# Performance work log

Measured on AMD Instinct MI355X. Metric: run time of the kernel, lower is better.

## Reference

```python
import jax, jax.numpy as jnp
import numpy as np

B, L, H, OUT = 128, 256, 512, 256


def setup_inputs() -> dict:
    key = jax.random.key(0)
    ks = jax.random.split(key, 13)
    s = 1.0 / np.sqrt(H)
    u = lambda k, shape: jax.random.uniform(k, shape, jnp.float32, -s, s)
    C = jax.random.normal(ks[0], (L, H), jnp.float32)
    # strictly increasing observation times per sample
    dt0 = jax.random.uniform(ks[1], (B, L, 1), jnp.float32)
    t = jnp.cumsum(dt0, axis=1)
    mask = jax.random.randint(ks[2], (B, L, H), 0, 2).astype(jnp.int32)
    # GRU-D parameters: fused gate weights [z | r | candidate]
    Wx = u(ks[3], (H, 3 * H))   # input -> gates
    Wh = u(ks[4], (H, 3 * H))   # hidden -> gates
    Wm = u(ks[5], (H, 3 * H))   # mask  -> gates
    b = u(ks[6], (3 * H,))
    w_gx = u(ks[7], (H,))       # diagonal input-decay weight
    b_gx = u(ks[8], (H,))
    W_gh = u(ks[9], (H, H))     # hidden-decay weight
    b_gh = u(ks[10], (H,))
    W_out = u(ks[11], (H, OUT))
    b_out = u(ks[12], (OUT,))
    return dict(C=C, t=t, mask=mask, Wx=Wx, Wh=Wh, Wm=Wm, b=b, w_gx=w_gx,
                b_gx=b_gx, W_gh=W_gh, b_gh=b_gh, W_out=W_out, b_out=b_out)


def _grud_decode(C, t, mask_f, Wx, Wh, Wm, b, w_gx, b_gx, W_gh, b_gh, W_out, b_out):
    Bn, Ln = t.shape[0], t.shape[1]
    Hn = C.shape[1]
    m = mask_f                                                     # (B,L,H) float 0/1
    tt = jnp.broadcast_to(t[:, :, 0:1], (Bn, Ln, Hn))              # (B,L,H)
    dt = tt - jnp.concatenate([tt[:, :1], tt[:, :-1]], axis=1)     # dt[:,0]=0
    x = jnp.broadcast_to(C[None], (Bn, Ln, Hn))
    # empirical mean of observed values per sample/feature
    x_mean = jnp.sum(m * x, axis=1) / jnp.maximum(jnp.sum(m, axis=1), 1.0)  # (B,H)

    def step(carry, inp):
        h, x_last, d_prev, m_prev = carry
        xi, mi, dti = inp                                          # xi:(H,), mi/dti:(B,H)
        # time since last observation (GRU-D delta recurrence)
        delta = dti + (1.0 - m_prev) * d_prev
        gamma_x = jnp.exp(-jnp.maximum(0.0, w_gx * delta + b_gx))  # input decay
        gamma_h = jnp.exp(-jnp.maximum(0.0, delta @ W_gh + b_gh))  # hidden decay
        x_hat = mi * xi + (1.0 - mi) * (gamma_x * x_last + (1.0 - gamma_x) * x_mean)
        h = gamma_h * h
        pre = x_hat @ Wx + mi @ Wm + b                             # (B,3H)
        zr = jax.nn.sigmoid(pre[:, :2 * Hn] + h @ Wh[:, :2 * Hn])
        z, r = zr[:, :Hn], zr[:, Hn:]
        h_tilde = jnp.tanh(pre[:, 2 * Hn:] + (r * h) @ Wh[:, 2 * Hn:])
        h_new = (1.0 - z) * h + z * h_tilde
        x_last = mi * xi + (1.0 - mi) * x_last
        return (h_new, x_last, delta, mi), h_new

    init = (jnp.zeros((Bn, Hn), C.dtype), x_mean,
            jnp.zeros((Bn, Hn), C.dtype), jnp.ones((Bn, Hn), C.dtype))
    xs = (C, jnp.transpose(m, (1, 0, 2)), jnp.transpose(dt, (1, 0, 2)))
    _, h_seq = jax.lax.scan(step, init, xs)                        # (L,B,H)
    h_seq = jnp.transpose(h_seq, (1, 0, 2))                        # (B,L,H) == permute(1,0,2)
    return h_seq @ W_out + b_out                                   # (B,L,OUT)


def reference(C, t, mask, Wx, Wh, Wm, b, w_gx, b_gx, W_gh, b_gh, W_out, b_out):
    return _grud_decode(C, t, mask.astype(C.dtype), Wx, Wh, Wm, b,
                        w_gx, b_gx, W_gh, b_gh, W_out, b_out)
```

## Files before the change

kernel.cpp:

```cpp
#include <hip/hip_runtime.h>
#include <hip/hip_bf16.h>
#include <hip/hip_fp16.h>
#include <stdint.h>

typedef short bf16x8 __attribute__((ext_vector_type(8)));
typedef unsigned short u16x8 __attribute__((ext_vector_type(8)));
typedef float f32x4  __attribute__((ext_vector_type(4)));
typedef __hip_bfloat16 bf16;
typedef unsigned long long u64;

#define MFMA16(a,b,c) __builtin_amdgcn_mfma_f32_16x16x32_bf16((a),(b),(c),0,0,0)

__device__ __forceinline__ float bf2f(bf16 x){ return __bfloat162float(x); }
__device__ __forceinline__ bf16  f2bf(float x){ return __float2bfloat16(x); }
__device__ __forceinline__ short f2bs(float x){ bf16 t = __float2bfloat16(x); return *(short*)&t; }
__device__ __forceinline__ float bs2f(short s){ bf16 t; *(short*)&t = s; return __bfloat162float(t); }
__device__ __forceinline__ float h2f(unsigned short u){ __half t; *(unsigned short*)&t = u; return __half2float(t); }
__device__ __forceinline__ float sf(float x){ return (fabsf(x) < 1e30f) ? x : 0.f; }

#define NB   128
#define NL   256
#define CH   32
#define MCH  4096
#define NQ   8


__global__ void build_wcatT(const float* __restrict__ Wx, const float* __restrict__ Wm,
                            bf16* __restrict__ dst) {
    int i = blockIdx.x * 256 + threadIdx.x;
    if (i >= 1536 * 1024) return;
    int n = i >> 10, k = i & 1023;
    float v = (k < 512) ? Wx[k * 1536 + n] : Wm[(k - 512) * 1536 + n];
    dst[i] = f2bf(sf(v));
}

__global__ void transpose_f2b(const float* __restrict__ src, bf16* __restrict__ dst,
                              int R, int C) {
    int i = blockIdx.x * 256 + threadIdx.x;
    if (i >= R * C) return;
    int r = i % R, c = i / R;
    dst[i] = f2bf(sf(src[r * C + c]));
}


__global__ void xmean_kernel(const int* __restrict__ mask, const float* __restrict__ Cmat,
                             float* __restrict__ xmean) {
    int g = blockIdx.x * 256 + threadIdx.x;
    int b = g >> 9, h = g & 511;
    float s = 0.f, cnt = 0.f;
    for (int l = 0; l < NL; ++l) {
        int m = mask[(size_t)((b << 8) + l) * 512 + h];
        if (m) { s += sf(Cmat[(l << 9) + h]); cnt += 1.f; }
    }
    xmean[g] = s / fmaxf(cnt, 1.f);
}

__global__ void prep_kernel(const int* __restrict__ mask, const float* __restrict__ Cmat,
                            const float* __restrict__ t_in,
                            const float* __restrict__ w_gx, const float* __restrict__ b_gx,
                            const float* __restrict__ xmean,
                            float* __restrict__ xlastC, float* __restrict__ dprevC,
                            float* __restrict__ mprevC, float* __restrict__ tprevC,
                            bf16* __restrict__ Xcat,
                            bf16* __restrict__ Dbuf,
                            int q) {
    int g = blockIdx.x * 256 + threadIdx.x;
    int b = g >> 9, h = g & 511;
    float wg = sf(w_gx[h]), bg = sf(b_gx[h]);
    float xm = xmean[g];
    float xlast, dprev, mprev, tprev;
    if (q == 0) { xlast = xm; dprev = 0.f; mprev = 1.f; tprev = 0.f; }
    else { xlast = xlastC[g]; dprev = dprevC[g]; mprev = mprevC[g]; tprev = tprevC[g]; }
    for (int ll = 0; ll < CH; ++ll) {
        int l = q * CH + ll;
        float tc = sf(t_in[(b << 8) + l]);
        float dtv = (l == 0) ? 0.f : (tc - tprev);
        tprev = tc;
        float mi = (float)mask[(size_t)((b << 8) + l) * 512 + h];
        float delta = dtv + (1.f - mprev) * dprev;
        float gx = __expf(-fmaxf(wg * delta + bg, 0.f));
        float xi = sf(Cmat[(l << 9) + h]);
        float xh = mi * xi + (1.f - mi) * (gx * xlast + (1.f - gx) * xm);
        size_t row = (size_t)ll * 128 + b;
        Xcat[row * 1024 + h]       = f2bf(xh);
        Xcat[row * 1024 + 512 + h] = f2bf(mi);
        Dbuf[row * 512 + h]        = f2bf(delta);
        xlast = mi * xi + (1.f - mi) * xlast;
        dprev = delta; mprev = mi;
    }
    xlastC[g] = xlast; dprevC[g] = dprev; mprevC[g] = mprev; tprevC[g] = tprev;
}

template <int MODE>
__global__ __launch_bounds__(256) void gemm_bt(const bf16* __restrict__ A,
                                               const bf16* __restrict__ BT,
                                               const float* __restrict__ bias,
                                               void* __restrict__ Cout,
                                               int N, int K, int q) {
    const int nb = N >> 7;
    int bn = blockIdx.x % nb, bm = blockIdx.x / nb;
    __shared__ bf16 As[4096];
    __shared__ bf16 Bs[4096];
    int tid = threadIdx.x, lane = tid & 63, w = tid >> 6;
    int wm = w >> 1, wn = w & 1;
    int quad = lane >> 4, l15 = lane & 15;
    f32x4 acc[4][4];
// ... 36 lines not shown
    int row0 = bm * 128 + wm * 64, col0 = bn * 128 + wn * 64;
    #pragma unroll
    for (int mt = 0; mt < 4; ++mt) {
        #pragma unroll
        for (int nt = 0; nt < 4; ++nt) {
            int col = col0 + nt * 16 + l15;
            float bvf = sf(bias[col]);
            #pragma unroll
            for (int r = 0; r < 4; ++r) {
                int row = row0 + mt * 16 + quad * 4 + r;
                float v = acc[mt][nt][r] + bvf;
                if (MODE == 1)
                    ((__half*)Cout)[(size_t)row * N + col] = __float2half(__expf(-fmaxf(v, 0.f)));
                else if (MODE == 2) {
                    int bb = row & 127, lloc = row >> 7;
                    ((float*)Cout)[(size_t)((bb << 8) + q * CH + lloc) * N + col] = v;
                } else
                    ((bf16*)Cout)[(size_t)row * N + col] = f2bf(v);
            }
        }
    }
}

__global__ __launch_bounds__(512, 1) void scan_kernel(
        const bf16* __restrict__ pre,
        const __half* __restrict__ gammaf,
        const bf16* __restrict__ WhT,
        bf16* __restrict__ hseq,
        float* __restrict__ hcarry,
        u64* __restrict__ rbuf,
        u64* __restrict__ hnbuf,
        unsigned* __restrict__ ctr) {
    int bx = blockIdx.x;
    int c = bx & 7, w = bx >> 3;
    int tid = threadIdx.x, lane = tid & 63, v = tid >> 6;
    int wi = (w << 3) | v;
    int quad = lane >> 4, l15 = lane & 15;
    __shared__ bf16 hb[16 * 520];
    __shared__ bf16 rh[16 * 520];

    bf16x8 whz[16], whr[16], whh[16];
    int col0 = wi * 16;
    #pragma unroll
    for (int kf = 0; kf < 16; ++kf) {
        int n = col0 + l15;
        whz[kf] = *(const bf16x8*)(WhT + (size_t)n * 512 + kf * 32 + quad * 8);
        whr[kf] = *(const bf16x8*)(WhT + (size_t)(512 + n) * 512 + kf * 32 + quad * 8);
        whh[kf] = *(const bf16x8*)(WhT + (size_t)(1024 + n) * 512 + kf * 32 + quad * 8);
    }

    u64* rclu = rbuf  + (size_t)c * 2048;
    u64* hclu = hnbuf + (size_t)c * 2048;
    const unsigned short* gus = (const unsigned short*)gammaf;
    unsigned* fA = ctr + c * 64;
    unsigned* fB = ctr + c * 64 + 32;

    for (int i = tid; i < 16 * 512; i += 512) {
        int row = i >> 9, col = i & 511;
        int brow = c * 16 + row;
        float g0 = __half2float(gammaf[(size_t)brow * 512 + col]);
        hb[row * 520 + col] = f2bf(hcarry[(size_t)brow * 512 + col] * g0);
    }
    float hfo[4];
    #pragma unroll
    for (int r = 0; r < 4; ++r) {
        int brow = c * 16 + quad * 4 + r;
        int cc = col0 + l15;
        float g0 = __half2float(gammaf[(size_t)brow * 512 + cc]);
        hfo[r] = hcarry[(size_t)brow * 512 + cc] * g0;
    }
    __syncthreads();

    int rrow = tid >> 5, rword = tid & 31;
    int prow = tid >> 5, pc16 = tid & 31, pcol = pc16 << 4, pregion = pc16 >> 3;

    for (int t = 0; t < CH; ++t) {
        unsigned ep = (unsigned)(t + 1);
        bool lastt = (t == CH - 1);
        float pz[4], prr[4], ph[4], gow[4];
        #pragma unroll
        for (int r = 0; r < 4; ++r) {
            int brow = c * 16 + quad * 4 + r;
            size_t pb = ((size_t)t * 128 + brow) * 1536;
            int cc = col0 + l15;
            pz[r]  = bf2f(pre[pb + cc]);
            prr[r] = bf2f(pre[pb + 512 + cc]);
            ph[r]  = bf2f(pre[pb + 1024 + cc]);
            gow[r] = lastt ? 1.f
                   : __half2float(gammaf[((size_t)(t + 1) * 128 + brow) * 512 + cc]);
        }
        u16x8 gt[2];
        {
            size_t gb = ((size_t)(lastt ? t : t + 1) * 128 + c * 16 + prow) * 512 + pcol;
            #pragma unroll
            for (int j = 0; j < 2; ++j) gt[j] = *(const u16x8*)(gus + gb + j * 8);
        }
        f32x4 az = (f32x4){0.f,0.f,0.f,0.f}, ar = az;
        #pragma unroll
        for (int kf = 0; kf < 16; ++kf) {
            bf16x8 a = *(const bf16x8*)&hb[l15 * 520 + kf * 32 + quad * 8];
            az = MFMA16(a, whz[kf], az);
            ar = MFMA16(a, whr[kf], ar);
        }
        float zv[4];
        #pragma unroll
        for (int r = 0; r < 4; ++r) {
            zv[r] = 1.f / (1.f + __expf(-(az[r] + pz[r])));
            float rv = 1.f / (1.f + __expf(-(ar[r] + prr[r])));
            rh[(quad * 4 + r) * 520 + col0 + l15] = f2bf(rv * hfo[r]);
        }
        __syncthreads();
        {
            u64 wv = *(const u64*)&rh[rrow * 520 + w * 128 + rword * 4];
            __hip_atomic_store(&rclu[rrow * 128 + w * 32 + rword], wv,
                               __ATOMIC_RELAXED, __HIP_MEMORY_SCOPE_AGENT);
        }
        __syncthreads();
        if (tid == 0) {
            __hip_atomic_store(&fA[w], ep, __ATOMIC_RELAXED, __HIP_MEMORY_SCOPE_AGENT);
            int guard = 0;
            for (;;) {
                bool ok = true;
                #pragma unroll
                for (int j = 0; j < 4; ++j)
                    ok &= (__hip_atomic_load(&fA[j], __ATOMIC_RELAXED,
                                             __HIP_MEMORY_SCOPE_AGENT) >= ep);
                if (ok || ++guard >= (1 << 16)) break;
                __builtin_amdgcn_s_sleep(1);
            }
        }
        __syncthreads();
        if (pregion != w) {
            #pragma unroll
            for (int j = 0; j < 4; ++j) {
                u64 wv = __hip_atomic_load(&rclu[prow * 128 + pc16 * 4 + j],
                                           __ATOMIC_RELAXED, __HIP_MEMORY_SCOPE_AGENT);
                *(u64*)&rh[prow * 520 + pcol + j * 4] = wv;
            }
        }
        __syncthreads();
        f32x4 ah = (f32x4){0.f,0.f,0.f,0.f};
        #pragma unroll
        for (int kf = 0; kf < 16; ++kf) {
            bf16x8 a = *(const bf16x8*)&rh[l15 * 520 + kf * 32 + quad * 8];
            ah = MFMA16(a, whh[kf], ah);
        }
        #pragma unroll
        for (int r = 0; r < 4; ++r) {
            int row = quad * 4 + r;
            int cc = col0 + l15;
            float x = ah[r] + ph[r];
            float e = __expf(-2.f * fabsf(x));
            float th = copysignf((1.f - e) / (1.f + e), x);
            float hn = (1.f - zv[r]) * hfo[r] + zv[r] * th;
            hb[row * 520 + cc] = f2bf(hn);
            if (lastt) {
                int brow = c * 16 + row;
                __builtin_nontemporal_store(hn, &hcarry[(size_t)brow * 512 + cc]);
            }
            hfo[r] = hn * gow[r];
        }
        __syncthreads();
        {
            u64 wv = *(const u64*)&hb[rrow * 520 + w * 128 + rword * 4];
            __hip_atomic_store(&hclu[rrow * 128 + w * 32 + rword], wv,
                               __ATOMIC_RELAXED, __HIP_MEMORY_SCOPE_AGENT);
        }
        __syncthreads();
        if (tid == 0) {
            __hip_atomic_store(&fB[w], ep, __ATOMIC_RELAXED, __HIP_MEMORY_SCOPE_AGENT);
            int guard = 0;
            for (;;) {
                bool ok = true;
                #pragma unroll
                for (int j = 0; j < 4; ++j)
                    ok &= (__hip_atomic_load(&fB[j], __ATOMIC_RELAXED,
                                             __HIP_MEMORY_SCOPE_AGENT) >= ep);
                if (ok || ++guard >= (1 << 16)) break;
                __builtin_amdgcn_s_sleep(1);
            }
        }
        __syncthreads();
        u64 hw[4];
        if (pregion != w) {
            #pragma unroll
            for (int j = 0; j < 4; ++j)
                hw[j] = __hip_atomic_load(&hclu[prow * 128 + pc16 * 4 + j],
                                          __ATOMIC_RELAXED, __HIP_MEMORY_SCOPE_AGENT);
        } else {
            #pragma unroll
            for (int j = 0; j < 4; ++j)
                hw[j] = *(const u64*)&hb[prow * 520 + pcol + j * 4];
        }
        if (w == 0) {
            int brow = c * 16 + prow;
            u64* hs = (u64*)&hseq[((size_t)t * 128 + brow) * 512 + pcol];
            #pragma unroll
            for (int j = 0; j < 4; ++j) __builtin_nontemporal_store(hw[j], &hs[j]);
        }
        #pragma unroll
        for (int j = 0; j < 4; ++j) {
            u16x8* gp = (u16x8*)&gt[0];
            short o4[4];
            #pragma unroll
            for (int e = 0; e < 4; ++e) {
                short hv = (short)((hw[j] >> (16 * e)) & 0xFFFF);
                float g = lastt ? 1.f : h2f(((unsigned short*)gp)[j * 4 + e]);
                o4[e] = f2bs(bs2f(hv) * g);
            }
            u64 ov = ((u64)(unsigned short)o4[0]) | ((u64)(unsigned short)o4[1] << 16)
                   | ((u64)(unsigned short)o4[2] << 32) | ((u64)(unsigned short)o4[3] << 48);
            *(u64*)&hb[prow * 520 + pcol + j * 4] = ov;
        }
        __syncthreads();
    }
}


extern "C" void kernel_launch(void* const* d_in, const int* in_sizes, int n_in,
                              void* d_out, int out_size, void* d_ws, size_t ws_size,
                              hipStream_t stream) {
    const float* C     = (const float*)d_in[0];
    const float* t_in  = (const float*)d_in[1];
    const int*   mask  = (const int*)d_in[2];
    const float* Wx    = (const float*)d_in[3];
    const float* Wh    = (const float*)d_in[4];
    const float* Wm    = (const float*)d_in[5];
    const float* bvec  = (const float*)d_in[6];
    const float* w_gx  = (const float*)d_in[7];
    const float* b_gx  = (const float*)d_in[8];
    const float* W_gh  = (const float*)d_in[9];
    const float* b_gh  = (const float*)d_in[10];
    const float* W_out = (const float*)d_in[11];
    const float* b_out = (const float*)d_in[12];

    char* w = (char*)d_ws;
    unsigned* ctr   = (unsigned*)(w + 0);
    float* hcarry   = (float*)(w + 16384);
    float* xmean    = (float*)(w + 278528);
    float* xlastC   = (float*)(w + 540672);
    float* dprevC   = (float*)(w + 802816);
    float* mprevC   = (float*)(w + 1064960);
    float* tprevC   = (float*)(w + 1327104);
    bf16*  wcatT    = (bf16*)(w + 1589248);
    bf16*  wghT     = (bf16*)(w + 4734976);
    bf16*  whT      = (bf16*)(w + 5259264);
    bf16*  woutT    = (bf16*)(w + 6832128);
    bf16*  Xcat     = (bf16*)(w + 7094272);
    bf16*  Dbuf     = (bf16*)(w + 15482880);
    bf16*  pre      = (bf16*)(w + 19677184);
    __half* gamma   = (__half*)(w + 32260096);
    bf16*  hseq     = (bf16*)(w + 36454400);
    u64*   rbuf     = (u64*)(w + 40648704);
    u64*   hnbuf    = (u64*)(w + 40779776);

    hipMemsetAsync(w, 0, 278528, stream);

    build_wcatT<<<6144, 256, 0, stream>>>(Wx, Wm, wcatT);
    transpose_f2b<<<1024, 256, 0, stream>>>(W_gh, wghT, 512, 512);
    transpose_f2b<<<3072, 256, 0, stream>>>(Wh, whT, 512, 1536);
    transpose_f2b<<<512, 256, 0, stream>>>(W_out, woutT, 512, 256);
    xmean_kernel<<<256, 256, 0, stream>>>(mask, C, xmean);

    for (int q = 0; q < NQ; ++q) {
        prep_kernel<<<256, 256, 0, stream>>>(mask, C, t_in, w_gx, b_gx, xmean,
                                             xlastC, dprevC, mprevC, tprevC,
                                             Xcat, Dbuf, q);
        gemm_bt<0><<<32 * 12, 256, 0, stream>>>(Xcat, wcatT, bvec, (void*)pre, 1536, 1024, q);
        gemm_bt<1><<<32 * 4, 256, 0, stream>>>(Dbuf, wghT, b_gh, (void*)gamma, 512, 512, q);
        scan_kernel<<<32, 512, 0, stream>>>(pre, gamma, whT, hseq, hcarry,
                                            rbuf, hnbuf, ctr + q * 512);
        gemm_bt<2><<<32 * 2, 256, 0, stream>>>(hseq, woutT, b_out, d_out, 256, 512, q);
    }
}
```

Baseline: 2.884 ms.

## Overlap cluster barrier waits with local z-gate and partial candidate MFMAs

The r-gate is now computed first so its exchange can be published early. While waiting on the cross-block flag, each block computes the z-gate MFMAs and the locally owned slice of the candidate matmul, so only the remote K-chunks remain after the barrier. The per-step loads of pre-activations and gamma for the next step are issued before the second barrier wait, and the local h-region rescale is done before the wait too. The intent is to hide inter-workgroup synchronisation latency behind useful compute, at the cost of more live registers and more complex control flow.

```diff
diff --git a/kernel.cpp b/kernel.cpp
--- a/kernel.cpp
+++ b/kernel.cpp
@@ -23,6 +23,8 @@
 #define CH   32
 #define MCH  4096
 #define NQ   8
+
+#define RLXA __ATOMIC_RELAXED, __HIP_MEMORY_SCOPE_AGENT
 
 
 __global__ void build_wcatT(const float* __restrict__ Wx, const float* __restrict__ Wm,
@@ -216,57 +218,70 @@
     int rrow = tid >> 5, rword = tid & 31;
     int prow = tid >> 5, pc16 = tid & 31, pcol = pc16 << 4, pregion = pc16 >> 3;
 
-    for (int t = 0; t < CH; ++t) {
-        unsigned ep = (unsigned)(t + 1);
-        bool lastt = (t == CH - 1);
-        float pz[4], prr[4], ph[4], gow[4];
+    float pz[4], prr[4], ph[4], gow[4];
+    u16x8 gt[2], gtn[2];
+    {
         #pragma unroll
         for (int r = 0; r < 4; ++r) {
             int brow = c * 16 + quad * 4 + r;
-            size_t pb = ((size_t)t * 128 + brow) * 1536;
+            size_t pb = (size_t)brow * 1536;
             int cc = col0 + l15;
             pz[r]  = bf2f(pre[pb + cc]);
             prr[r] = bf2f(pre[pb + 512 + cc]);
             ph[r]  = bf2f(pre[pb + 1024 + cc]);
-            gow[r] = lastt ? 1.f
-                   : __half2float(gammaf[((size_t)(t + 1) * 128 + brow) * 512 + cc]);
-        }
-        u16x8 gt[2];
+            gow[r] = __half2float(gammaf[((size_t)128 + brow) * 512 + cc]);
+        }
+        size_t gb = ((size_t)128 + c * 16 + prow) * 512 + pcol;
+        gt[0] = *(const u16x8*)(gus + gb);
+        gt[1] = *(const u16x8*)(gus + gb + 8);
+    }
+
+    for (int t = 0; t < CH; ++t) {
+        unsigned ep = (unsigned)(t + 1);
+        bool lastt = (t == CH - 1);
+
+        f32x4 ar = (f32x4){0.f,0.f,0.f,0.f};
+        #pragma unroll
+        for (int kf = 0; kf < 16; ++kf) {
+            bf16x8 a = *(const bf16x8*)&hb[l15 * 520 + kf * 32 + quad * 8];
+            ar = MFMA16(a, whr[kf], ar);
+        }
+        #pragma unroll
+        for (int r = 0; r < 4; ++r) {
+            float rv = 1.f / (1.f + __expf(-(ar[r] + prr[r])));
+            rh[(quad * 4 + r) * 520 + col0 + l15] = f2bf(rv * hfo[r]);
+        }
+        __syncthreads();
         {
-            size_t gb = ((size_t)(lastt ? t : t + 1) * 128 + c * 16 + prow) * 512 + pcol;
-            #pragma unroll
-            for (int j = 0; j < 2; ++j) gt[j] = *(const u16x8*)(gus + gb + j * 8);
-        }
-        f32x4 az = (f32x4){0.f,0.f,0.f,0.f}, ar = az;
+            u64 wv = *(const u64*)&rh[rrow * 520 + w * 128 + rword * 4];
+            __hip_atomic_store(&rclu[rrow * 128 + w * 32 + rword], wv, RLXA);
+        }
+        __syncthreads();
+        if (tid == 0) __hip_atomic_store(&fA[w], ep, RLXA);
+        f32x4 az = (f32x4){0.f,0.f,0.f,0.f};
         #pragma unroll
         for (int kf = 0; kf < 16; ++kf) {
             bf16x8 a = *(const bf16x8*)&hb[l15 * 520 + kf * 32 + quad * 8];
             az = MFMA16(a, whz[kf], az);
-            ar = MFMA16(a, whr[kf], ar);
+        }
+        f32x4 ah = (f32x4){0.f,0.f,0.f,0.f};
+        #pragma unroll
+        for (int kq = 0; kq < 4; ++kq) {
+            int kf = w * 4 + kq;
+            bf16x8 a = *(const bf16x8*)&rh[l15 * 520 + kf * 32 + quad * 8];
+            ah = MFMA16(a, whh[kf], ah);
         }
         float zv[4];
         #pragma unroll
-        for (int r = 0; r < 4; ++r) {
+        for (int r = 0; r < 4; ++r)
             zv[r] = 1.f / (1.f + __expf(-(az[r] + pz[r])));
-            float rv = 1.f / (1.f + __expf(-(ar[r] + prr[r])));
-            rh[(quad * 4 + r) * 520 + col0 + l15] = f2bf(rv * hfo[r]);
-        }
-        __syncthreads();
-        {
-            u64 wv = *(const u64*)&rh[rrow * 520 + w * 128 + rword * 4];
-            __hip_atomic_store(&rclu[rrow * 128 + w * 32 + rword], wv,
-                               __ATOMIC_RELAXED, __HIP_MEMORY_SCOPE_AGENT);
-        }
-        __syncthreads();
         if (tid == 0) {
-            __hip_atomic_store(&fA[w], ep, __ATOMIC_RELAXED, __HIP_MEMORY_SCOPE_AGENT);
             int guard = 0;
             for (;;) {
                 bool ok = true;
                 #pragma unroll
                 for (int j = 0; j < 4; ++j)
-                    ok &= (__hip_atomic_load(&fA[j], __ATOMIC_RELAXED,
-                                             __HIP_MEMORY_SCOPE_AGENT) >= ep);
+                    ok &= (__hip_atomic_load(&fA[j], RLXA) >= ep);
                 if (ok || ++guard >= (1 << 16)) break;
                 __builtin_amdgcn_s_sleep(1);
             }
@@ -275,15 +290,14 @@
         if (pregion != w) {
             #pragma unroll
             for (int j = 0; j < 4; ++j) {
-                u64 wv = __hip_atomic_load(&rclu[prow * 128 + pc16 * 4 + j],
-                                           __ATOMIC_RELAXED, __HIP_MEMORY_SCOPE_AGENT);
+                u64 wv = __hip_atomic_load(&rclu[prow * 128 + pc16 * 4 + j], RLXA);
                 *(u64*)&rh[prow * 520 + pcol + j * 4] = wv;
             }
         }
         __syncthreads();
-        f32x4 ah = (f32x4){0.f,0.f,0.f,0.f};
         #pragma unroll
         for (int kf = 0; kf < 16; ++kf) {
+            if ((kf >> 2) == w) continue;
             bf16x8 a = *(const bf16x8*)&rh[l15 * 520 + kf * 32 + quad * 8];
             ah = MFMA16(a, whh[kf], ah);
         }
@@ -305,56 +319,99 @@
         __syncthreads();
         {
             u64 wv = *(const u64*)&hb[rrow * 520 + w * 128 + rword * 4];
-            __hip_atomic_store(&hclu[rrow * 128 + w * 32 + rword], wv,
-                               __ATOMIC_RELAXED, __HIP_MEMORY_SCOPE_AGENT);
-        }
-        __syncthreads();
+            __hip_atomic_store(&hclu[rrow * 128 + w * 32 + rword], wv, RLXA);
+        }
+        __syncthreads();
+        if (tid == 0) __hip_atomic_store(&fB[w], ep, RLXA);
+        if (pregion == w) {
+            u64 h0 = *(const u64*)&hb[prow * 520 + pcol + 0];
+            u64 h1 = *(const u64*)&hb[prow * 520 + pcol + 4];
+            u64 h2 = *(const u64*)&hb[prow * 520 + pcol + 8];
+            u64 h3 = *(const u64*)&hb[prow * 520 + pcol + 12];
+            if (w == 0) {
+                int brow = c * 16 + prow;
+                u64* hs = (u64*)&hseq[((size_t)t * 128 + brow) * 512 + pcol];
+                __builtin_nontemporal_store(h0, &hs[0]);
+                __builtin_nontemporal_store(h1, &hs[1]);
+                __builtin_nontemporal_store(h2, &hs[2]);
+                __builtin_nontemporal_store(h3, &hs[3]);
+            }
+            const unsigned short* gtu = (const unsigned short*)&gt[0];
+            u64 hwv[4] = {h0, h1, h2, h3};
+            #pragma unroll
+            for (int j = 0; j < 4; ++j) {
+                short o4[4];
+                #pragma unroll
+                for (int e = 0; e < 4; ++e) {
+                    short hv = (short)((hwv[j] >> (16 * e)) & 0xFFFF);
+                    float g = lastt ? 1.f : h2f(gtu[j * 4 + e]);
+                    o4[e] = f2bs(bs2f(hv) * g);
+                }
+                u64 ov = ((u64)(unsigned short)o4[0]) | ((u64)(unsigned short)o4[1] << 16)
+                       | ((u64)(unsigned short)o4[2] << 32) | ((u64)(unsigned short)o4[3] << 48);
+                *(u64*)&hb[prow * 520 + pcol + j * 4] = ov;
+            }
+        }
+        if (!lastt) {
+            int tn = t + 1; bool lastn = (tn == CH - 1);
+            #pragma unroll
+            for (int r = 0; r < 4; ++r) {
+                int brow = c * 16 + quad * 4 + r;
+                size_t pb = ((size_t)tn * 128 + brow) * 1536;
+                int cc = col0 + l15;
+                pz[r]  = bf2f(pre[pb + cc]);
+                prr[r] = bf2f(pre[pb + 512 + cc]);
+                ph[r]  = bf2f(pre[pb + 1024 + cc]);
+                gow[r] = lastn ? 1.f
+                       : __half2float(gammaf[((size_t)(tn + 1) * 128 + brow) * 512 + cc]);
+            }
+            size_t gb = ((size_t)(lastn ? tn : tn + 1) * 128 + c * 16 + prow) * 512 + pcol;
+            gtn[0] = *(const u16x8*)(gus + gb);
+            gtn[1] = *(const u16x8*)(gus + gb + 8);
+        }
         if (tid == 0) {
-            __hip_atomic_store(&fB[w], ep, __ATOMIC_RELAXED, __HIP_MEMORY_SCOPE_AGENT);
             int guard = 0;
             for (;;) {
                 bool ok = true;
                 #pragma unroll
                 for (int j = 0; j < 4; ++j)
-                    ok &= (__hip_atomic_load(&fB[j], __ATOMIC_RELAXED,
-                                             __HIP_MEMORY_SCOPE_AGENT) >= ep);
+                    ok &= (__hip_atomic_load(&fB[j], RLXA) >= ep);
                 if (ok || ++guard >= (1 << 16)) break;
                 __builtin_amdgcn_s_sleep(1);
             }
         }
         __syncthreads();
-        u64 hw[4];
         if (pregion != w) {
-            #pragma unroll
-            for (int j = 0; j < 4; ++j)
-                hw[j] = __hip_atomic_load(&hclu[prow * 128 + pc16 * 4 + j],
-                                          __ATOMIC_RELAXED, __HIP_MEMORY_SCOPE_AGENT);
-        } else {
-            #pragma unroll
-            for (int j = 0; j < 4; ++j)
-                hw[j] = *(const u64*)&hb[prow * 520 + pcol + j * 4];
-        }
-        if (w == 0) {
-            int brow = c * 16 + prow;
-            u64* hs = (u64*)&hseq[((size_t)t * 128 + brow) * 512 + pcol];
-            #pragma unroll
-            for (int j = 0; j < 4; ++j) __builtin_nontemporal_store(hw[j], &hs[j]);
-        }
-        #pragma unroll
-        for (int j = 0; j < 4; ++j) {
-            u16x8* gp = (u16x8*)&gt[0];
-            short o4[4];
-            #pragma unroll
-            for (int e = 0; e < 4; ++e) {
-                short hv = (short)((hw[j] >> (16 * e)) & 0xFFFF);
-                float g = lastt ? 1.f : h2f(((unsigned short*)gp)[j * 4 + e]);
-                o4[e] = f2bs(bs2f(hv) * g);
-            }
-            u64 ov = ((u64)(unsigned short)o4[0]) | ((u64)(unsigned short)o4[1] << 16)
-                   | ((u64)(unsigned short)o4[2] << 32) | ((u64)(unsigned short)o4[3] << 48);
-            *(u64*)&hb[prow * 520 + pcol + j * 4] = ov;
-        }
-        __syncthreads();
+            u64 h0 = __hip_atomic_load(&hclu[prow * 128 + pc16 * 4 + 0], RLXA);
+            u64 h1 = __hip_atomic_load(&hclu[prow * 128 + pc16 * 4 + 1], RLXA);
+            u64 h2 = __hip_atomic_load(&hclu[prow * 128 + pc16 * 4 + 2], RLXA);
+            u64 h3 = __hip_atomic_load(&hclu[prow * 128 + pc16 * 4 + 3], RLXA);
+            if (w == 0) {
+                int brow = c * 16 + prow;
+                u64* hs = (u64*)&hseq[((size_t)t * 128 + brow) * 512 + pcol];
+                __builtin_nontemporal_store(h0, &hs[0]);
+                __builtin_nontemporal_store(h1, &hs[1]);
+                __builtin_nontemporal_store(h2, &hs[2]);
+                __builtin_nontemporal_store(h3, &hs[3]);
+            }
+            const unsigned short* gtu = (const unsigned short*)&gt[0];
+            u64 hwv[4] = {h0, h1, h2, h3};
+            #pragma unroll
+            for (int j = 0; j < 4; ++j) {
+                short o4[4];
+                #pragma unroll
+                for (int e = 0; e < 4; ++e) {
+                    short hv = (short)((hwv[j] >> (16 * e)) & 0xFFFF);
+                    float g = lastt ? 1.f : h2f(gtu[j * 4 + e]);
+                    o4[e] = f2bs(bs2f(hv) * g);
+                }
+                u64 ov = ((u64)(unsigned short)o4[0]) | ((u64)(unsigned short)o4[1] << 16)
+                       | ((u64)(unsigned short)o4[2] << 32) | ((u64)(unsigned short)o4[3] << 48);
+                *(u64*)&hb[prow * 520 + pcol + j * 4] = ov;
+            }
+        }
+        __syncthreads();
+        if (!lastt) { gt[0] = gtn[0]; gt[1] = gtn[1]; }
     }
 }
 
```

Result: slower. 3.326 ms (+15.3%).

## Hoist full-sequence prep and GEMMs out of chunk loop; swizzle LDS layout

Applied to the files above, without the earlier changes.

When the workspace is large enough, the input prep, the gate GEMM, the decay GEMM and the output GEMM each run once over all 256 timesteps instead of in 8 chunks. The scan kernel then runs per chunk over the full-size buffers. This cuts launch count and gives the GEMMs far larger grids. The shared-memory h/rh tiles also move from padded row-major to a blocked layout that matches the MFMA operand reads, aiming to cut LDS bank conflicts. The fast path needs about 275 MB of workspace and falls back to the chunked path otherwise.

```diff
diff --git a/kernel.cpp b/kernel.cpp
--- a/kernel.cpp
+++ b/kernel.cpp
@@ -21,8 +21,13 @@
 #define NB   128
 #define NL   256
 #define CH   32
-#define MCH  4096
 #define NQ   8
+
+#define RLXA __ATOMIC_RELAXED, __HIP_MEMORY_SCOPE_AGENT
+
+__device__ __forceinline__ int lx(int row, int col) {
+    return ((col >> 5) << 9) | (((col >> 3) & 3) << 7) | (row << 3) | (col & 7);
+}
 
 
 __global__ void build_wcatT(const float* __restrict__ Wx, const float* __restrict__ Wm,
@@ -63,7 +68,7 @@
                             float* __restrict__ mprevC, float* __restrict__ tprevC,
                             bf16* __restrict__ Xcat,
                             bf16* __restrict__ Dbuf,
-                            int q) {
+                            int q, int nsteps) {
     int g = blockIdx.x * 256 + threadIdx.x;
     int b = g >> 9, h = g & 511;
     float wg = sf(w_gx[h]), bg = sf(b_gx[h]);
@@ -71,7 +76,7 @@
     float xlast, dprev, mprev, tprev;
     if (q == 0) { xlast = xm; dprev = 0.f; mprev = 1.f; tprev = 0.f; }
     else { xlast = xlastC[g]; dprev = dprevC[g]; mprev = mprevC[g]; tprev = tprevC[g]; }
-    for (int ll = 0; ll < CH; ++ll) {
+    for (int ll = 0; ll < nsteps; ++ll) {
         int l = q * CH + ll;
         float tc = sf(t_in[(b << 8) + l]);
         float dtv = (l == 0) ? 0.f : (tc - tprev);
@@ -178,8 +183,8 @@
     int tid = threadIdx.x, lane = tid & 63, v = tid >> 6;
     int wi = (w << 3) | v;
     int quad = lane >> 4, l15 = lane & 15;
-    __shared__ bf16 hb[16 * 520];
-    __shared__ bf16 rh[16 * 520];
+    __shared__ bf16 hb[8192];
+    __shared__ bf16 rh[8192];
 
     bf16x8 whz[16], whr[16], whh[16];
     int col0 = wi * 16;
@@ -201,7 +206,7 @@
         int row = i >> 9, col = i & 511;
         int brow = c * 16 + row;
         float g0 = __half2float(gammaf[(size_t)brow * 512 + col]);
-        hb[row * 520 + col] = f2bf(hcarry[(size_t)brow * 512 + col] * g0);
+        hb[lx(row, col)] = f2bf(hcarry[(size_t)brow * 512 + col] * g0);
     }
     float hfo[4];
     #pragma unroll
@@ -214,6 +219,8 @@
     __syncthreads();
 
     int rrow = tid >> 5, rword = tid & 31;
+    int rcol = w * 128 + rword * 4;
+    int rsrc = lx(rrow, rcol);
     int prow = tid >> 5, pc16 = tid & 31, pcol = pc16 << 4, pregion = pc16 >> 3;
 
     for (int t = 0; t < CH; ++t) {
@@ -240,7 +247,7 @@
         f32x4 az = (f32x4){0.f,0.f,0.f,0.f}, ar = az;
         #pragma unroll
         for (int kf = 0; kf < 16; ++kf) {
-            bf16x8 a = *(const bf16x8*)&hb[l15 * 520 + kf * 32 + quad * 8];
+            bf16x8 a = *(const bf16x8*)&hb[(kf << 9) | (quad << 7) | (l15 << 3)];
             az = MFMA16(a, whz[kf], az);
             ar = MFMA16(a, whr[kf], ar);
         }
@@ -249,24 +256,22 @@
         for (int r = 0; r < 4; ++r) {
             zv[r] = 1.f / (1.f + __expf(-(az[r] + pz[r])));
             float rv = 1.f / (1.f + __expf(-(ar[r] + prr[r])));
-            rh[(quad * 4 + r) * 520 + col0 + l15] = f2bf(rv * hfo[r]);
+            rh[lx(quad * 4 + r, col0 + l15)] = f2bf(rv * hfo[r]);
         }
         __syncthreads();
         {
-            u64 wv = *(const u64*)&rh[rrow * 520 + w * 128 + rword * 4];
-            __hip_atomic_store(&rclu[rrow * 128 + w * 32 + rword], wv,
-                               __ATOMIC_RELAXED, __HIP_MEMORY_SCOPE_AGENT);
+            u64 wv = *(const u64*)&rh[rsrc];
+            __hip_atomic_store(&rclu[rrow * 128 + w * 32 + rword], wv, RLXA);
         }
         __syncthreads();
         if (tid == 0) {
-            __hip_atomic_store(&fA[w], ep, __ATOMIC_RELAXED, __HIP_MEMORY_SCOPE_AGENT);
+            __hip_atomic_store(&fA[w], ep, RLXA);
             int guard = 0;
             for (;;) {
                 bool ok = true;
                 #pragma unroll
                 for (int j = 0; j < 4; ++j)
-                    ok &= (__hip_atomic_load(&fA[j], __ATOMIC_RELAXED,
-                                             __HIP_MEMORY_SCOPE_AGENT) >= ep);
+                    ok &= (__hip_atomic_load(&fA[j], RLXA) >= ep);
                 if (ok || ++guard >= (1 << 16)) break;
                 __builtin_amdgcn_s_sleep(1);
             }
@@ -275,16 +280,15 @@
         if (pregion != w) {
             #pragma unroll
             for (int j = 0; j < 4; ++j) {
-                u64 wv = __hip_atomic_load(&rclu[prow * 128 + pc16 * 4 + j],
-                                           __ATOMIC_RELAXED, __HIP_MEMORY_SCOPE_AGENT);
-                *(u64*)&rh[prow * 520 + pcol + j * 4] = wv;
+                u64 wv = __hip_atomic_load(&rclu[prow * 128 + pc16 * 4 + j], RLXA);
+                *(u64*)&rh[lx(prow, pcol + j * 4)] = wv;
             }
         }
         __syncthreads();
         f32x4 ah = (f32x4){0.f,0.f,0.f,0.f};
         #pragma unroll
         for (int kf = 0; kf < 16; ++kf) {
-            bf16x8 a = *(const bf16x8*)&rh[l15 * 520 + kf * 32 + quad * 8];
+            bf16x8 a = *(const bf16x8*)&rh[(kf << 9) | (quad << 7) | (l15 << 3)];
             ah = MFMA16(a, whh[kf], ah);
         }
         #pragma unroll
@@ -295,7 +299,7 @@
             float e = __expf(-2.f * fabsf(x));
             float th = copysignf((1.f - e) / (1.f + e), x);
             float hn = (1.f - zv[r]) * hfo[r] + zv[r] * th;
-            hb[row * 520 + cc] = f2bf(hn);
+            hb[lx(row, cc)] = f2bf(hn);
             if (lastt) {
                 int brow = c * 16 + row;
                 __builtin_nontemporal_store(hn, &hcarry[(size_t)brow * 512 + cc]);
@@ -304,20 +308,18 @@
         }
         __syncthreads();
         {
-            u64 wv = *(const u64*)&hb[rrow * 520 + w * 128 + rword * 4];
-            __hip_atomic_store(&hclu[rrow * 128 + w * 32 + rword], wv,
-                               __ATOMIC_RELAXED, __HIP_MEMORY_SCOPE_AGENT);
+            u64 wv = *(const u64*)&hb[rsrc];
+            __hip_atomic_store(&hclu[rrow * 128 + w * 32 + rword], wv, RLXA);
         }
         __syncthreads();
         if (tid == 0) {
-            __hip_atomic_store(&fB[w], ep, __ATOMIC_RELAXED, __HIP_MEMORY_SCOPE_AGENT);
+            __hip_atomic_store(&fB[w], ep, RLXA);
             int guard = 0;
             for (;;) {
                 bool ok = true;
                 #pragma unroll
                 for (int j = 0; j < 4; ++j)
-                    ok &= (__hip_atomic_load(&fB[j], __ATOMIC_RELAXED,
-                                             __HIP_MEMORY_SCOPE_AGENT) >= ep);
+                    ok &= (__hip_atomic_load(&fB[j], RLXA) >= ep);
                 if (ok || ++guard >= (1 << 16)) break;
                 __builtin_amdgcn_s_sleep(1);
             }
@@ -327,12 +329,11 @@
         if (pregion != w) {
             #pragma unroll
             for (int j = 0; j < 4; ++j)
-                hw[j] = __hip_atomic_load(&hclu[prow * 128 + pc16 * 4 + j],
-                                          __ATOMIC_RELAXED, __HIP_MEMORY_SCOPE_AGENT);
+                hw[j] = __hip_atomic_load(&hclu[prow * 128 + pc16 * 4 + j], RLXA);
         } else {
             #pragma unroll
             for (int j = 0; j < 4; ++j)
-                hw[j] = *(const u64*)&hb[prow * 520 + pcol + j * 4];
+                hw[j] = *(const u64*)&hb[lx(prow, pcol + j * 4)];
         }
         if (w == 0) {
             int brow = c * 16 + prow;
@@ -352,7 +353,7 @@
             }
             u64 ov = ((u64)(unsigned short)o4[0]) | ((u64)(unsigned short)o4[1] << 16)
                    | ((u64)(unsigned short)o4[2] << 32) | ((u64)(unsigned short)o4[3] << 48);
-            *(u64*)&hb[prow * 520 + pcol + j * 4] = ov;
+            *(u64*)&hb[lx(prow, pcol + j * 4)] = ov;
         }
         __syncthreads();
     }
@@ -388,13 +389,6 @@
     bf16*  wghT     = (bf16*)(w + 4734976);
     bf16*  whT      = (bf16*)(w + 5259264);
     bf16*  woutT    = (bf16*)(w + 6832128);
-    bf16*  Xcat     = (bf16*)(w + 7094272);
-    bf16*  Dbuf     = (bf16*)(w + 15482880);
-    bf16*  pre      = (bf16*)(w + 19677184);
-    __half* gamma   = (__half*)(w + 32260096);
-    bf16*  hseq     = (bf16*)(w + 36454400);
-    u64*   rbuf     = (u64*)(w + 40648704);
-    u64*   hnbuf    = (u64*)(w + 40779776);
 
     hipMemsetAsync(w, 0, 278528, stream);
 
@@ -404,14 +398,47 @@
     transpose_f2b<<<512, 256, 0, stream>>>(W_out, woutT, 512, 256);
     xmean_kernel<<<256, 256, 0, stream>>>(mask, C, xmean);
 
-    for (int q = 0; q < NQ; ++q) {
+    const size_t BIG_NEEDED = 275791872ull;
+    if (ws_size >= BIG_NEEDED) {
+        bf16*  XcatF  = (bf16*)(w + 7094272);
+        bf16*  DbufF  = (bf16*)(w + 74203136);
+        bf16*  preF   = (bf16*)(w + 107757568);
+        __half* gamF  = (__half*)(w + 208420864);
+        bf16*  hseqF  = (bf16*)(w + 241975296);
+        u64*   rbuf   = (u64*)(w + 275529728);
+        u64*   hnbuf  = (u64*)(w + 275660800);
+
         prep_kernel<<<256, 256, 0, stream>>>(mask, C, t_in, w_gx, b_gx, xmean,
                                              xlastC, dprevC, mprevC, tprevC,
-                                             Xcat, Dbuf, q);
-        gemm_bt<0><<<32 * 12, 256, 0, stream>>>(Xcat, wcatT, bvec, (void*)pre, 1536, 1024, q);
-        gemm_bt<1><<<32 * 4, 256, 0, stream>>>(Dbuf, wghT, b_gh, (void*)gamma, 512, 512, q);
-        scan_kernel<<<32, 512, 0, stream>>>(pre, gamma, whT, hseq, hcarry,
-                                            rbuf, hnbuf, ctr + q * 512);
-        gemm_bt<2><<<32 * 2, 256, 0, stream>>>(hseq, woutT, b_out, d_out, 256, 512, q);
-    }
-}
+                                             XcatF, DbufF, 0, NL);
+        gemm_bt<0><<<256 * 12, 256, 0, stream>>>(XcatF, wcatT, bvec, (void*)preF, 1536, 1024, 0);
+        gemm_bt<1><<<256 * 4, 256, 0, stream>>>(DbufF, wghT, b_gh, (void*)gamF, 512, 512, 0);
+        for (int q = 0; q < NQ; ++q) {
+            scan_kernel<<<32, 512, 0, stream>>>(preF + (size_t)q * 4096 * 1536,
+                                                gamF + (size_t)q * 4096 * 512,
+                                                whT,
+                                                hseqF + (size_t)q * 4096 * 512,
+                                                hcarry, rbuf, hnbuf, ctr + q * 512);
+        }
+        gemm_bt<2><<<256 * 2, 256, 0, stream>>>(hseqF, woutT, b_out, d_out, 256, 512, 0);
+    } else {
+        bf16*  Xcat   = (bf16*)(w + 7094272);
+        bf16*  Dbuf   = (bf16*)(w + 15482880);
+        bf16*  pre    = (bf16*)(w + 19677184);
+        __half* gamma = (__half*)(w + 32260096);
+        bf16*  hseq   = (bf16*)(w + 36454400);
+        u64*   rbuf   = (u64*)(w + 40648704);
+        u64*   hnbuf  = (u64*)(w + 40779776);
+
+        for (int q = 0; q < NQ; ++q) {
+            prep_kernel<<<256, 256, 0, stream>>>(mask, C, t_in, w_gx, b_gx, xmean,
+                                                 xlastC, dprevC, mprevC, tprevC,
+                                                 Xcat, Dbuf, q, CH);
+            gemm_bt<0><<<32 * 12, 256, 0, stream>>>(Xcat, wcatT, bvec, (void*)pre, 1536, 1024, q);
+            gemm_bt<1><<<32 * 4, 256, 0, stream>>>(Dbuf, wghT, b_gh, (void*)gamma, 512, 512, q);
+            scan_kernel<<<32, 512, 0, stream>>>(pre, gamma, whT, hseq, hcarry,
+                                                rbuf, hnbuf, ctr + q * 512);
+            gemm_bt<2><<<32 * 2, 256, 0, stream>>>(hseq, woutT, b_out, d_out, 256, 512, q);
+        }
+    }
+}
```

Result: slower. 3.192 ms (+10.7%).

## Interleave two batch groups per scan block to hide cross-block flag waits

Applied to the files above, without the earlier changes.

Each scan workgroup now processes two 16-row batch groups (X and Y) instead of one, with the grid halved from 32 to 16 blocks. Phases of the two groups are interleaved so that while one group waits on the inter-block flag exchange for r*h or h_new, the other group's MFMA work and stores proceed. This is meant to hide the latency of the spin-wait synchronisation across the 4 column-split blocks. In exchange, each block does twice the sequential work, uses twice the LDS and more registers, and the flag layout changes.

```diff
diff --git a/kernel.cpp b/kernel.cpp
--- a/kernel.cpp
+++ b/kernel.cpp
@@ -23,6 +23,8 @@
 #define CH   32
 #define MCH  4096
 #define NQ   8
+
+#define RLXA __ATOMIC_RELAXED, __HIP_MEMORY_SCOPE_AGENT
 
 
 __global__ void build_wcatT(const float* __restrict__ Wx, const float* __restrict__ Wm,
@@ -174,12 +176,14 @@
         u64* __restrict__ hnbuf,
         unsigned* __restrict__ ctr) {
     int bx = blockIdx.x;
-    int c = bx & 7, w = bx >> 3;
+    int c = bx & 3, w = bx >> 2;
     int tid = threadIdx.x, lane = tid & 63, v = tid >> 6;
     int wi = (w << 3) | v;
     int quad = lane >> 4, l15 = lane & 15;
-    __shared__ bf16 hb[16 * 520];
-    __shared__ bf16 rh[16 * 520];
+    __shared__ bf16 hbX[16 * 520];
+    __shared__ bf16 rhX[16 * 520];
+    __shared__ bf16 hbY[16 * 520];
+    __shared__ bf16 rhY[16 * 520];
 
     bf16x8 whz[16], whr[16], whh[16];
     int col0 = wi * 16;
@@ -191,25 +195,34 @@
         whh[kf] = *(const bf16x8*)(WhT + (size_t)(1024 + n) * 512 + kf * 32 + quad * 8);
     }
 
-    u64* rclu = rbuf  + (size_t)c * 2048;
-    u64* hclu = hnbuf + (size_t)c * 2048;
+    u64* rcluX = rbuf  + (size_t)(c * 2 + 0) * 2048;
+    u64* rcluY = rbuf  + (size_t)(c * 2 + 1) * 2048;
+    u64* hcluX = hnbuf + (size_t)(c * 2 + 0) * 2048;
+    u64* hcluY = hnbuf + (size_t)(c * 2 + 1) * 2048;
     const unsigned short* gus = (const unsigned short*)gammaf;
-    unsigned* fA = ctr + c * 64;
-    unsigned* fB = ctr + c * 64 + 32;
+    unsigned* fAX = ctr + c * 128;
+    unsigned* fAY = ctr + c * 128 + 8;
+    unsigned* fBX = ctr + c * 128 + 16;
+    unsigned* fBY = ctr + c * 128 + 24;
+    int rowX0 = c * 32, rowY0 = c * 32 + 16;
 
     for (int i = tid; i < 16 * 512; i += 512) {
         int row = i >> 9, col = i & 511;
-        int brow = c * 16 + row;
-        float g0 = __half2float(gammaf[(size_t)brow * 512 + col]);
-        hb[row * 520 + col] = f2bf(hcarry[(size_t)brow * 512 + col] * g0);
-    }
-    float hfo[4];
+        int bX = rowX0 + row, bY = rowY0 + row;
+        hbX[row * 520 + col] = f2bf(hcarry[(size_t)bX * 512 + col]
+                                    * __half2float(gammaf[(size_t)bX * 512 + col]));
+        hbY[row * 520 + col] = f2bf(hcarry[(size_t)bY * 512 + col]
+                                    * __half2float(gammaf[(size_t)bY * 512 + col]));
+    }
+    float hfoX[4], hfoY[4];
     #pragma unroll
     for (int r = 0; r < 4; ++r) {
-        int brow = c * 16 + quad * 4 + r;
+        int bX = rowX0 + quad * 4 + r, bY = rowY0 + quad * 4 + r;
         int cc = col0 + l15;
-        float g0 = __half2float(gammaf[(size_t)brow * 512 + cc]);
-        hfo[r] = hcarry[(size_t)brow * 512 + cc] * g0;
+        hfoX[r] = hcarry[(size_t)bX * 512 + cc]
+                * __half2float(gammaf[(size_t)bX * 512 + cc]);
+        hfoY[r] = hcarry[(size_t)bY * 512 + cc]
+                * __half2float(gammaf[(size_t)bY * 512 + cc]);
     }
     __syncthreads();
 
@@ -219,54 +232,82 @@
     for (int t = 0; t < CH; ++t) {
         unsigned ep = (unsigned)(t + 1);
         bool lastt = (t == CH - 1);
-        float pz[4], prr[4], ph[4], gow[4];
+        float pzX[4], prrX[4], phX[4], gowX[4];
+        float pzY[4], prrY[4], phY[4], gowY[4];
         #pragma unroll
         for (int r = 0; r < 4; ++r) {
-            int brow = c * 16 + quad * 4 + r;
-            size_t pb = ((size_t)t * 128 + brow) * 1536;
+            int bX = rowX0 + quad * 4 + r, bY = rowY0 + quad * 4 + r;
             int cc = col0 + l15;
-            pz[r]  = bf2f(pre[pb + cc]);
-            prr[r] = bf2f(pre[pb + 512 + cc]);
-            ph[r]  = bf2f(pre[pb + 1024 + cc]);
-            gow[r] = lastt ? 1.f
-                   : __half2float(gammaf[((size_t)(t + 1) * 128 + brow) * 512 + cc]);
-        }
-        u16x8 gt[2];
-        {
-            size_t gb = ((size_t)(lastt ? t : t + 1) * 128 + c * 16 + prow) * 512 + pcol;
-            #pragma unroll
-            for (int j = 0; j < 2; ++j) gt[j] = *(const u16x8*)(gus + gb + j * 8);
-        }
-        f32x4 az = (f32x4){0.f,0.f,0.f,0.f}, ar = az;
+            size_t pbX = ((size_t)t * 128 + bX) * 1536;
+            size_t pbY = ((size_t)t * 128 + bY) * 1536;
+            pzX[r]  = bf2f(pre[pbX + cc]);
+            prrX[r] = bf2f(pre[pbX + 512 + cc]);
+            phX[r]  = bf2f(pre[pbX + 1024 + cc]);
+            pzY[r]  = bf2f(pre[pbY + cc]);
+            prrY[r] = bf2f(pre[pbY + 512 + cc]);
+            phY[r]  = bf2f(pre[pbY + 1024 + cc]);
+            gowX[r] = lastt ? 1.f
+                    : __half2float(gammaf[((size_t)(t + 1) * 128 + bX) * 512 + cc]);
+            gowY[r] = lastt ? 1.f
+                    : __half2float(gammaf[((size_t)(t + 1) * 128 + bY) * 512 + cc]);
+        }
+        u16x8 gtX[2], gtY[2];
+        {
+            size_t gstep = (size_t)(lastt ? t : t + 1) * 128;
+            size_t gbX = (gstep + rowX0 + prow) * 512 + pcol;
+            size_t gbY = (gstep + rowY0 + prow) * 512 + pcol;
+            gtX[0] = *(const u16x8*)(gus + gbX); gtX[1] = *(const u16x8*)(gus + gbX + 8);
+            gtY[0] = *(const u16x8*)(gus + gbY); gtY[1] = *(const u16x8*)(gus + gbY + 8);
+        }
+        f32x4 azX = (f32x4){0.f,0.f,0.f,0.f}, arX = azX;
         #pragma unroll
         for (int kf = 0; kf < 16; ++kf) {
-            bf16x8 a = *(const bf16x8*)&hb[l15 * 520 + kf * 32 + quad * 8];
-            az = MFMA16(a, whz[kf], az);
-            ar = MFMA16(a, whr[kf], ar);
-        }
-        float zv[4];
+            bf16x8 a = *(const bf16x8*)&hbX[l15 * 520 + kf * 32 + quad * 8];
+            azX = MFMA16(a, whz[kf], azX);
+            arX = MFMA16(a, whr[kf], arX);
+        }
+        float zvX[4];
         #pragma unroll
         for (int r = 0; r < 4; ++r) {
-            zv[r] = 1.f / (1.f + __expf(-(az[r] + pz[r])));
-            float rv = 1.f / (1.f + __expf(-(ar[r] + prr[r])));
-            rh[(quad * 4 + r) * 520 + col0 + l15] = f2bf(rv * hfo[r]);
-        }
-        __syncthreads();
-        {
-            u64 wv = *(const u64*)&rh[rrow * 520 + w * 128 + rword * 4];
-            __hip_atomic_store(&rclu[rrow * 128 + w * 32 + rword], wv,
-                               __ATOMIC_RELAXED, __HIP_MEMORY_SCOPE_AGENT);
-        }
-        __syncthreads();
+            zvX[r] = 1.f / (1.f + __expf(-(azX[r] + pzX[r])));
+            float rv = 1.f / (1.f + __expf(-(arX[r] + prrX[r])));
+            rhX[(quad * 4 + r) * 520 + col0 + l15] = f2bf(rv * hfoX[r]);
+        }
+        __syncthreads();
+        {
+            u64 wv = *(const u64*)&rhX[rrow * 520 + w * 128 + rword * 4];
+            __hip_atomic_store(&rcluX[rrow * 128 + w * 32 + rword], wv, RLXA);
+        }
+        __syncthreads();
+        if (tid == 0) __hip_atomic_store(&fAX[w], ep, RLXA);
+        f32x4 azY = (f32x4){0.f,0.f,0.f,0.f}, arY = azY;
+        #pragma unroll
+        for (int kf = 0; kf < 16; ++kf) {
+            bf16x8 a = *(const bf16x8*)&hbY[l15 * 520 + kf * 32 + quad * 8];
+            azY = MFMA16(a, whz[kf], azY);
+            arY = MFMA16(a, whr[kf], arY);
+        }
+        float zvY[4];
+        #pragma unroll
+        for (int r = 0; r < 4; ++r) {
+            zvY[r] = 1.f / (1.f + __expf(-(azY[r] + pzY[r])));
+            float rv = 1.f / (1.f + __expf(-(arY[r] + prrY[r])));
+            rhY[(quad * 4 + r) * 520 + col0 + l15] = f2bf(rv * hfoY[r]);
+        }
+        __syncthreads();
+        {
+            u64 wv = *(const u64*)&rhY[rrow * 520 + w * 128 + rword * 4];
+            __hip_atomic_store(&rcluY[rrow * 128 + w * 32 + rword], wv, RLXA);
+        }
+        __syncthreads();
+        if (tid == 0) __hip_atomic_store(&fAY[w], ep, RLXA);
         if (tid == 0) {
-            __hip_atomic_store(&fA[w], ep, __ATOMIC_RELAXED, __HIP_MEMORY_SCOPE_AGENT);
             int guard = 0;
             for (;;) {
                 bool ok = true;
                 #pragma unroll
                 for (int j = 0; j < 4; ++j)
-                    ok &= (__hip_atomic_load(&fA[j], __ATOMIC_RELAXED,
-                                             __HIP_MEMORY_SCOPE_AGENT) >= ep);
+                    ok &= (__hip_atomic_load(&fAX[j], RLXA) >= ep);
                 if (ok || ++guard >= (1 << 16)) break;
                 __builtin_amdgcn_s_sleep(1);
             }
@@ -275,84 +316,170 @@
         if (pregion != w) {
             #pragma unroll
             for (int j = 0; j < 4; ++j) {
-                u64 wv = __hip_atomic_load(&rclu[prow * 128 + pc16 * 4 + j],
-                                           __ATOMIC_RELAXED, __HIP_MEMORY_SCOPE_AGENT);
-                *(u64*)&rh[prow * 520 + pcol + j * 4] = wv;
-            }
-        }
-        __syncthreads();
-        f32x4 ah = (f32x4){0.f,0.f,0.f,0.f};
+                u64 wv = __hip_atomic_load(&rcluX[prow * 128 + pc16 * 4 + j], RLXA);
+                *(u64*)&rhX[prow * 520 + pcol + j * 4] = wv;
+            }
+        }
+        __syncthreads();
+        f32x4 ahX = (f32x4){0.f,0.f,0.f,0.f};
         #pragma unroll
         for (int kf = 0; kf < 16; ++kf) {
-            bf16x8 a = *(const bf16x8*)&rh[l15 * 520 + kf * 32 + quad * 8];
-            ah = MFMA16(a, whh[kf], ah);
+            bf16x8 a = *(const bf16x8*)&rhX[l15 * 520 + kf * 32 + quad * 8];
+            ahX = MFMA16(a, whh[kf], ahX);
         }
         #pragma unroll
         for (int r = 0; r < 4; ++r) {
             int row = quad * 4 + r;
             int cc = col0 + l15;
-            float x = ah[r] + ph[r];
+            float x = ahX[r] + phX[r];
             float e = __expf(-2.f * fabsf(x));
             float th = copysignf((1.f - e) / (1.f + e), x);
-            float hn = (1.f - zv[r]) * hfo[r] + zv[r] * th;
-            hb[row * 520 + cc] = f2bf(hn);
-            if (lastt) {
-                int brow = c * 16 + row;
-                __builtin_nontemporal_store(hn, &hcarry[(size_t)brow * 512 + cc]);
-            }
-            hfo[r] = hn * gow[r];
-        }
-        __syncthreads();
-        {
-            u64 wv = *(const u64*)&hb[rrow * 520 + w * 128 + rword * 4];
-            __hip_atomic_store(&hclu[rrow * 128 + w * 32 + rword], wv,
-                               __ATOMIC_RELAXED, __HIP_MEMORY_SCOPE_AGENT);
-        }
-        __syncthreads();
+            float hn = (1.f - zvX[r]) * hfoX[r] + zvX[r] * th;
+            hbX[row * 520 + cc] = f2bf(hn);
+            if (lastt)
+                __builtin_nontemporal_store(hn, &hcarry[(size_t)(rowX0 + row) * 512 + cc]);
+            hfoX[r] = hn * gowX[r];
+        }
+        __syncthreads();
+        {
+            u64 wv = *(const u64*)&hbX[rrow * 520 + w * 128 + rword * 4];
+            __hip_atomic_store(&hcluX[rrow * 128 + w * 32 + rword], wv, RLXA);
+        }
+        __syncthreads();
+        if (tid == 0) __hip_atomic_store(&fBX[w], ep, RLXA);
         if (tid == 0) {
-            __hip_atomic_store(&fB[w], ep, __ATOMIC_RELAXED, __HIP_MEMORY_SCOPE_AGENT);
             int guard = 0;
             for (;;) {
                 bool ok = true;
                 #pragma unroll
                 for (int j = 0; j < 4; ++j)
-                    ok &= (__hip_atomic_load(&fB[j], __ATOMIC_RELAXED,
-                                             __HIP_MEMORY_SCOPE_AGENT) >= ep);
+                    ok &= (__hip_atomic_load(&fAY[j], RLXA) >= ep);
                 if (ok || ++guard >= (1 << 16)) break;
                 __builtin_amdgcn_s_sleep(1);
             }
         }
         __syncthreads();
-        u64 hw[4];
         if (pregion != w) {
             #pragma unroll
-            for (int j = 0; j < 4; ++j)
-                hw[j] = __hip_atomic_load(&hclu[prow * 128 + pc16 * 4 + j],
-                                          __ATOMIC_RELAXED, __HIP_MEMORY_SCOPE_AGENT);
-        } else {
+            for (int j = 0; j < 4; ++j) {
+                u64 wv = __hip_atomic_load(&rcluY[prow * 128 + pc16 * 4 + j], RLXA);
+                *(u64*)&rhY[prow * 520 + pcol + j * 4] = wv;
+            }
+        }
+        __syncthreads();
+        f32x4 ahY = (f32x4){0.f,0.f,0.f,0.f};
+        #pragma unroll
+        for (int kf = 0; kf < 16; ++kf) {
+            bf16x8 a = *(const bf16x8*)&rhY[l15 * 520 + kf * 32 + quad * 8];
+            ahY = MFMA16(a, whh[kf], ahY);
+        }
+        #pragma unroll
+        for (int r = 0; r < 4; ++r) {
+            int row = quad * 4 + r;
+            int cc = col0 + l15;
+            float x = ahY[r] + phY[r];
+            float e = __expf(-2.f * fabsf(x));
+            float th = copysignf((1.f - e) / (1.f + e), x);
+            float hn = (1.f - zvY[r]) * hfoY[r] + zvY[r] * th;
+            hbY[row * 520 + cc] = f2bf(hn);
+            if (lastt)
+                __builtin_nontemporal_store(hn, &hcarry[(size_t)(rowY0 + row) * 512 + cc]);
+            hfoY[r] = hn * gowY[r];
+        }
+        __syncthreads();
+        {
+            u64 wv = *(const u64*)&hbY[rrow * 520 + w * 128 + rword * 4];
+            __hip_atomic_store(&hcluY[rrow * 128 + w * 32 + rword], wv, RLXA);
+        }
+        __syncthreads();
+        if (tid == 0) __hip_atomic_store(&fBY[w], ep, RLXA);
+        if (tid == 0) {
+            int guard = 0;
+            for (;;) {
+                bool ok = true;
+                #pragma unroll
+                for (int j = 0; j < 4; ++j)
+                    ok &= (__hip_atomic_load(&fBX[j], RLXA) >= ep);
+                if (ok || ++guard >= (1 << 16)) break;
+                __builtin_amdgcn_s_sleep(1);
+            }
+        }
+        __syncthreads();
+        {
+            u64 hw[4];
+            if (pregion != w) {
+                #pragma unroll
+                for (int j = 0; j < 4; ++j)
+                    hw[j] = __hip_atomic_load(&hcluX[prow * 128 + pc16 * 4 + j], RLXA);
+            } else {
+                #pragma unroll
+                for (int j = 0; j < 4; ++j)
+                    hw[j] = *(const u64*)&hbX[prow * 520 + pcol + j * 4];
+            }
+            if (w == 0) {
+                int brow = rowX0 + prow;
+                u64* hs = (u64*)&hseq[((size_t)t * 128 + brow) * 512 + pcol];
+                #pragma unroll
+                for (int j = 0; j < 4; ++j) __builtin_nontemporal_store(hw[j], &hs[j]);
+            }
+            const unsigned short* gtu = (const unsigned short*)&gtX[0];
             #pragma unroll
-            for (int j = 0; j < 4; ++j)
-                hw[j] = *(const u64*)&hb[prow * 520 + pcol + j * 4];
-        }
-        if (w == 0) {
-            int brow = c * 16 + prow;
-            u64* hs = (u64*)&hseq[((size_t)t * 128 + brow) * 512 + pcol];
+            for (int j = 0; j < 4; ++j) {
+                short o4[4];
+                #pragma unroll
+                for (int e = 0; e < 4; ++e) {
+                    short hv = (short)((hw[j] >> (16 * e)) & 0xFFFF);
+                    float g = lastt ? 1.f : h2f(gtu[j * 4 + e]);
+                    o4[e] = f2bs(bs2f(hv) * g);
+                }
+                u64 ov = ((u64)(unsigned short)o4[0]) | ((u64)(unsigned short)o4[1] << 16)
+                       | ((u64)(unsigned short)o4[2] << 32) | ((u64)(unsigned short)o4[3] << 48);
+                *(u64*)&hbX[prow * 520 + pcol + j * 4] = ov;
+            }
+        }
+        if (tid == 0) {
+            int guard = 0;
+            for (;;) {
+                bool ok = true;
+                #pragma unroll
+                for (int j = 0; j < 4; ++j)
+                    ok &= (__hip_atomic_load(&fBY[j], RLXA) >= ep);
+                if (ok || ++guard >= (1 << 16)) break;
+                __builtin_amdgcn_s_sleep(1);
+            }
+        }
+        __syncthreads();
+        {
+            u64 hw[4];
+            if (pregion != w) {
+                #pragma unroll
+                for (int j = 0; j < 4; ++j)
+                    hw[j] = __hip_atomic_load(&hcluY[prow * 128 + pc16 * 4 + j], RLXA);
+            } else {
+                #pragma unroll
+                for (int j = 0; j < 4; ++j)
+                    hw[j] = *(const u64*)&hbY[prow * 520 + pcol + j * 4];
+            }
+            if (w == 0) {
+                int brow = rowY0 + prow;
+                u64* hs = (u64*)&hseq[((size_t)t * 128 + brow) * 512 + pcol];
+                #pragma unroll
+                for (int j = 0; j < 4; ++j) __builtin_nontemporal_store(hw[j], &hs[j]);
+            }
+            const unsigned short* gtu = (const unsigned short*)&gtY[0];
             #pragma unroll
-            for (int j = 0; j < 4; ++j) __builtin_nontemporal_store(hw[j], &hs[j]);
-        }
-        #pragma unroll
-        for (int j = 0; j < 4; ++j) {
-            u16x8* gp = (u16x8*)&gt[0];
-            short o4[4];
-            #pragma unroll
-            for (int e = 0; e < 4; ++e) {
-                short hv = (short)((hw[j] >> (16 * e)) & 0xFFFF);
-                float g = lastt ? 1.f : h2f(((unsigned short*)gp)[j * 4 + e]);
-                o4[e] = f2bs(bs2f(hv) * g);
-            }
-            u64 ov = ((u64)(unsigned short)o4[0]) | ((u64)(unsigned short)o4[1] << 16)
-                   | ((u64)(unsigned short)o4[2] << 32) | ((u64)(unsigned short)o4[3] << 48);
-            *(u64*)&hb[prow * 520 + pcol + j * 4] = ov;
+            for (int j = 0; j < 4; ++j) {
+                short o4[4];
+                #pragma unroll
+                for (int e = 0; e < 4; ++e) {
+                    short hv = (short)((hw[j] >> (16 * e)) & 0xFFFF);
+                    float g = lastt ? 1.f : h2f(gtu[j * 4 + e]);
+                    o4[e] = f2bs(bs2f(hv) * g);
+                }
+                u64 ov = ((u64)(unsigned short)o4[0]) | ((u64)(unsigned short)o4[1] << 16)
+                       | ((u64)(unsigned short)o4[2] << 32) | ((u64)(unsigned short)o4[3] << 48);
+                *(u64*)&hbY[prow * 520 + pcol + j * 4] = ov;
+            }
         }
         __syncthreads();
     }
@@ -410,7 +537,7 @@
                                              Xcat, Dbuf, q);
         gemm_bt<0><<<32 * 12, 256, 0, stream>>>(Xcat, wcatT, bvec, (void*)pre, 1536, 1024, q);
         gemm_bt<1><<<32 * 4, 256, 0, stream>>>(Dbuf, wghT, b_gh, (void*)gamma, 512, 512, q);
-        scan_kernel<<<32, 512, 0, stream>>>(pre, gamma, whT, hseq, hcarry,
+        scan_kernel<<<16, 512, 0, stream>>>(pre, gamma, whT, hseq, hcarry,
                                             rbuf, hnbuf, ctr + q * 512);
         gemm_bt<2><<<32 * 2, 256, 0, stream>>>(hseq, woutT, b_out, d_out, 256, 512, q);
     }
```

Result: slower. 5.398 ms (+87.2%).
